# Performance work log

Hardware: AMD Instinct MI355X
Metric: run time of the kernel (lower is better)

## Reference

```python
import jax, jax.numpy as jnp
import numpy as np

B, C, N, T, Hd, L, F = 128, 8, 256, 64, 256, 2, 32  # batch, conv_channels, num_nodes(=hidden), obs_len, hidden, num_layers, filter_num


def setup_inputs() -> dict:
    key = jax.random.key(0)
    ks = jax.random.split(key, 20)
    s = 0.05
    f32 = jnp.float32
    return {
        "x": jax.random.normal(ks[0], (B, C, N, T), f32),
        "wst": jax.random.normal(ks[1], (C,), f32) * s,            # st_conv 1x1 weight
        "bst": jax.random.normal(ks[2], (1,), f32) * s,
        "Wh": jax.random.normal(ks[3], (Hd, N), f32) * s,           # hidden Linear
        "bh": jax.random.normal(ks[4], (Hd,), f32) * s,
        "Wih": jax.random.normal(ks[5], (4 * Hd, Hd), f32) * s,     # LSTM
        "Whh": jax.random.normal(ks[6], (4 * Hd, Hd), f32) * s,
        "bih": jax.random.normal(ks[7], (4 * Hd,), f32) * s,
        "bhh": jax.random.normal(ks[8], (4 * Hd,), f32) * s,
        "Wd": jax.random.normal(ks[9], (Hd, 2 * Hd), f32) * s,      # den Linear(2h->h)
        "bd": jax.random.normal(ks[10], (Hd,), f32) * s,
        "Wc": jax.random.normal(ks[11], (F, T), f32) * s,           # attention conv kernel (filter_num,1,obs_len,1) squeezed
        "bc": jax.random.normal(ks[12], (F,), f32) * s,
        "Wl1": jax.random.normal(ks[13], (F, 2 * Hd), f32) * s,     # attention linear1
        "bl1": jax.random.normal(ks[14], (F,), f32) * s,
        "Wl2": jax.random.normal(ks[15], (Hd, 2 * Hd + F), f32) * s,  # attention linear2
        "bl2": jax.random.normal(ks[16], (Hd,), f32) * s,
        "wend": jax.random.normal(ks[17], (C,), f32) * s,           # end_conv 1x1 weight
        "bend": jax.random.normal(ks[18], (C,), f32) * s,
    }


def _forward(x, wst, bst, Wh, bh, Wih, Whh, bih, bhh, Wd, bd, Wc, bc, Wl1, bl1, Wl2, bl2, wend, bend):
    b = x.shape[0]
    # st_conv (1x1 over channels) + relu, then (B, obs_len, num_nodes)
    y = jax.nn.relu(jnp.einsum("bcnt,c->bnt", x, wst) + bst[0])
    xcon = jax.nn.relu(jnp.einsum("bnt,hn->bth", y, Wh) + bh)  # (B, T, Hd)

    def lstm_cell(xt, ht, ct):
        g = xt @ Wih.T + bih + ht @ Whh.T + bhh
        i, f, gg, o = jnp.split(g, 4, axis=1)
        c2 = jax.nn.sigmoid(f) * ct + jax.nn.sigmoid(i) * jnp.tanh(gg)
        h2 = jax.nn.sigmoid(o) * jnp.tanh(c2)
        return h2, c2

    def attention(Hbuf, htt2):
        # Hbuf: (b, T, Hd); htt2: (b, 2Hd)
        w = htt2 @ Wl1.T + bl1                                   # (b, F)
        cv = jax.nn.relu(jnp.einsum("bto,ft->bof", Hbuf, Wc) + bc)  # (b, Hd, F)
        alpha = jax.nn.sigmoid(jnp.sum(cv * w[:, None, :], axis=2))  # (b, Hd)
        v = jnp.sum(alpha[:, :, None] * cv, axis=1)              # (b, F)
        return jax.nn.relu(jnp.concatenate([htt2, v], axis=1)) @ Wl2.T + bl2

    def step(carry, xt):
        ht, ct, attn_out, Hbuf = carry
        xi = xt
        new_ht = attn_out
        for _ in range(L):
            xd = jnp.concatenate([xi, attn_out], axis=1) @ Wd.T + bd
            ht, ct = lstm_cell(xd, ht, ct)
            htt2 = jnp.concatenate([ct, ht], axis=1)             # (b, 2Hd)
            new_ht = attention(Hbuf, htt2)                       # (b, Hd)
            output = jnp.concatenate([ht, new_ht], axis=1) @ Wd.T + bd
            Hbuf = jax.nn.relu(jnp.concatenate([Hbuf[:, 1:, :], output[:, None, :]], axis=1))
            attn_out = new_ht
            xi = output
        return (ht, ct, attn_out, Hbuf), new_ht

    z = jnp.zeros((b, Hd), x.dtype)
    carry0 = (z, z, z, jnp.zeros((b, T, Hd), x.dtype))
    _, res = jax.lax.scan(step, carry0, jnp.transpose(xcon, (1, 0, 2)))  # (T, b, Hd)
    r = jax.nn.relu(jnp.transpose(res, (1, 2, 0)))              # (b, Hd, T)
    # end_conv 1x1: (b, C, Hd, T)
    return r[:, None, :, :] * wend[None, :, None, None] + bend[None, :, None, None]


def reference(x, wst, bst, Wh, bh, Wih, Whh, bih, bhh, Wd, bd, Wc, bc, Wl1, bl1, Wl2, bl2, wend, bend):
    return _forward(x, wst, bst, Wh, bh, Wih, Whh, bih, bhh, Wd, bd, Wc, bc, Wl1, bl1, Wl2, bl2, wend, bend)
```

## Files before the change

kernel.cpp:

```cpp
#include <hip/hip_runtime.h>
#include <hip/hip_bf16.h>

typedef unsigned int uint;
typedef unsigned short ushort;
typedef __fp16 half2_t __attribute__((ext_vector_type(2)));

__device__ __forceinline__ ushort f16b(float x){
  return __builtin_bit_cast(ushort, (_Float16)x);
}
__device__ __forceinline__ uint pk_rne(float a, float b){
  return (uint)f16b(a) | ((uint)f16b(b) << 16);
}
__device__ __forceinline__ void pk_hl(float a, float b, uint& h, uint& l){
  _Float16 ha = (_Float16)a, hb = (_Float16)b;
  float la = (a - (float)ha) * 2048.f;
  float lb = (b - (float)hb) * 2048.f;
  h = (uint)__builtin_bit_cast(ushort, ha) | ((uint)__builtin_bit_cast(ushort, hb) << 16);
  l = pk_rne(la, lb);
}
__device__ __forceinline__ float fdot2(uint a, uint b, float c){
#if __has_builtin(__builtin_amdgcn_fdot2)
  return __builtin_amdgcn_fdot2(__builtin_bit_cast(half2_t, a),
                                __builtin_bit_cast(half2_t, b), c, false);
#else
  half2_t ha = __builtin_bit_cast(half2_t, a), hb = __builtin_bit_cast(half2_t, b);
  return c + (float)ha.x*(float)hb.x + (float)ha.y*(float)hb.y;
#endif
}
__device__ __forceinline__ float f16sel(uint p, uint hi){
  ushort us = hi ? (ushort)(p >> 16) : (ushort)(p & 0xffffu);
  return (float)__builtin_bit_cast(_Float16, us);
}
__device__ __forceinline__ float sigm(float x){ return 1.0f/(1.0f+__expf(-x)); }
__device__ __forceinline__ float tanh_(float x){
  x = fminf(fmaxf(x, -15.f), 15.f);
  float e = __expf(-2.f*x);
  return (1.f-e)/(1.f+e);
}
#define LO_SCALE (1.0f/2048.0f)


__global__ void kPack(const float* __restrict__ Wd, const float* __restrict__ Wih,
                      const float* __restrict__ Whh, const float* __restrict__ Wl1,
                      const float* __restrict__ Wl2, const float* __restrict__ Wc,
                      const float* __restrict__ Wh,  const float* __restrict__ bih,
                      const float* __restrict__ bhh,
                      uint4* __restrict__ Wd4, uint4* __restrict__ Wc4hi,
                      uint4* __restrict__ Wc4lo, uint4* __restrict__ Wl24,
                      float* __restrict__ Wl1f, uint* __restrict__ Wcrot,
                      uint* __restrict__ WhT2, float* __restrict__ bcomb)
{
  const int NTOT = 32768 + 65536 + 34816 + 16384 + 65536 + 32768 + 1024;
  for (int idx = blockIdx.x*blockDim.x + threadIdx.x; idx < NTOT; idx += gridDim.x*blockDim.x){
    int i = idx;
    if (i < 32768){
      int kpp=i>>8, o=i&255, k0=4*kpp;
      uint h0,l0,h1,l1;
      pk_hl(Wd[o*512+k0],   Wd[o*512+k0+1], h0,l0);
      pk_hl(Wd[o*512+k0+2], Wd[o*512+k0+3], h1,l1);
      Wd4[i] = make_uint4(h0,l0,h1,l1); continue; }
    i -= 32768;
    if (i < 65536){
      int kp=i>>8, hh=i&255;
      uint wh[4], wl[4];
      #pragma unroll
      for (int gi=0; gi<4; gi++){
        int row = gi*256+hh;
        float a,b;
        if (kp<128){ a=Wih[row*256+2*kp]; b=Wih[row*256+2*kp+1]; }
        else       { a=Whh[row*256+2*(kp-128)]; b=Whh[row*256+2*(kp-128)+1]; }
        pk_hl(a,b,wh[gi],wl[gi]);
      }
      Wc4hi[i] = make_uint4(wh[0],wh[1],wh[2],wh[3]);
      Wc4lo[i] = make_uint4(wl[0],wl[1],wl[2],wl[3]); continue; }
    i -= 65536;
    if (i < 34816){
      int kpp=i>>8, o=i&255, k0=4*kpp;
      uint h0,l0,h1,l1;
      pk_hl(Wl2[o*544+k0],   Wl2[o*544+k0+1], h0,l0);
      pk_hl(Wl2[o*544+k0+2], Wl2[o*544+k0+3], h1,l1);
      Wl24[i] = make_uint4(h0,l0,h1,l1); continue; }
    i -= 34816;
    if (i < 16384){ int kk=i>>5, f=i&31; Wl1f[i] = Wl1[f*512+kk]; continue; }
    i -= 16384;
    if (i < 65536){ int bb=i>>10, r=i&1023, ps=r>>5, f=r&31;
      float lo = Wc[f*64 + ((2*ps   - bb) & 63)];
      float hi = Wc[f*64 + ((2*ps+1 - bb) & 63)];
      Wcrot[i] = pk_rne(lo, hi); continue; }
    i -= 65536;
    if (i < 32768){ int np=i>>8, h=i&255;
      WhT2[i] = pk_rne(Wh[h*256+2*np], Wh[h*256+2*np+1]); continue; }
    i -= 32768;
    bcomb[i] = bih[i] + bhh[i];
  }
}

__global__ void k1a(const float* __restrict__ x, const float* __restrict__ wst,
                    const float* __restrict__ bst, ushort* __restrict__ yT)
{
  int b = blockIdx.x, tq = blockIdx.y, n = threadIdx.x;
  float acc[16];
  #pragma unroll
  for (int k=0;k<16;k++) acc[k]=0.f;
  for (int c=0;c<8;c++){
    const float4* xp = (const float4*)(x + ((size_t)((b*8+c)*256 + n)*64 + tq*16));
    float wc = wst[c];
    #pragma unroll
    for (int q=0;q<4;q++){
      float4 v = xp[q];
      acc[4*q+0] += v.x*wc; acc[4*q+1] += v.y*wc;
      acc[4*q+2] += v.z*wc; acc[4*q+3] += v.w*wc;
    }
  }
  float b0 = bst[0];
  #pragma unroll
  for (int k=0;k<16;k++){
    float v = fmaxf(acc[k]+b0, 0.f);
    yT[(size_t)(b*64 + tq*16 + k)*256 + n] = f16b(v);
  }
}

__global__ void k1b(const uint* __restrict__ yT2, const uint* __restrict__ WhT2,
                    const float* __restrict__ bh, float* __restrict__ xcon)
{
  __shared__ uint yp[8192];
  int b = blockIdx.x, tid = threadIdx.x;
  for (int i = tid; i < 8192; i += 256) yp[i] = yT2[(size_t)b*8192 + i];
  __syncthreads();
  int h = tid;
  float bias = bh[h];
  for (int tq=0;tq<4;tq++){
    float acc[16];
    #pragma unroll
    for (int k=0;k<16;k++) acc[k]=0.f;
    for (int np=0;np<128;np++){
      uint w2 = WhT2[np*256 + h];
      #pragma unroll
      for (int k=0;k<16;k++)
        acc[k] = fdot2(yp[(tq*16+k)*128 + np], w2, acc[k]);
    }
    #pragma unroll
    for (int k=0;k<16;k++)
      xcon[(size_t)(b*64 + tq*16 + k)*256 + h] = fmaxf(acc[k]+bias, 0.f);
  }
}

__global__ __launch_bounds__(512, 1)
void TPALSTM_17205638987874_kernel(const float* __restrict__ xcon,
        const uint4* __restrict__ Wd4, const uint4* __restrict__ Wc4hi,
        const uint4* __restrict__ Wc4lo, const uint4* __restrict__ Wl24,
        const float* __restrict__ Wl1f, const uint* __restrict__ Wcrot,
        const float* __restrict__ bd, const float* __restrict__ bcomb,
        const float* __restrict__ bl1, const float* __restrict__ bl2,
        const float* __restrict__ bc, float* __restrict__ res)
{
  __shared__ uint  Hp[32][256];
  __shared__ uint  cvp[256][17];
  __shared__ float gp[8][256];
  __shared__ float p2[2][256];
  __shared__ float ht[256], ct[256], alpha[256], nh[256];
  __shared__ __align__(16) uint2 APR2[288];
  __shared__ uint  wpair[16];

  int b = blockIdx.x, tid = threadIdx.x;
  int g = tid >> 8, o = tid & 255;

  for (int i = tid; i < 32*256; i += 512) ((uint*)Hp)[i] = 0u;
  if (tid < 256){ ht[tid]=0.f; ct[tid]=0.f; }
  if (tid >= 128 && tid < 256) APR2[tid] = make_uint2(0u,0u);
  __syncthreads();

  int base = 0;
  for (int t=0;t<64;t++){
    if (tid < 128){
      const float* xr = xcon + (size_t)(b*64+t)*256;
      uint h,l; pk_hl(xr[2*tid], xr[2*tid+1], h, l);
      APR2[tid] = make_uint2(h,l);
    }
    __syncthreads();

    for (int l=0;l<2;l++){
      {
        float ahi=0.f, alo=0.f;
        const uint4* wp = Wd4 + (size_t)(g*64)*256 + o;
        const uint4* ap = (const uint4*)(APR2 + g*128);
        #pragma unroll 4
        for (int kpp=0;kpp<64;kpp++){
          uint4 w = wp[0]; wp += 256;
          uint4 A = ap[kpp];
          ahi = fdot2(A.x, w.x, ahi); alo = fdot2(A.y, w.x, alo); alo = fdot2(A.x, w.y, alo);
          ahi = fdot2(A.z, w.z, ahi); alo = fdot2(A.w, w.z, alo); alo = fdot2(A.z, w.w, alo);
        }
        p2[g][o] = ahi + alo*LO_SCALE;
      }
      __syncthreads();
      if (tid < 128){
        float x0 = p2[0][2*tid]  + p2[1][2*tid]  + bd[2*tid];
        float x1 = p2[0][2*tid+1]+ p2[1][2*tid+1]+ bd[2*tid+1];
        uint h,l; pk_hl(x0,x1,h,l); APR2[tid]=make_uint2(h,l);
      } else if (tid < 256){
        int j=tid-128; uint h,l; pk_hl(ht[2*j], ht[2*j+1], h, l); APR2[tid]=make_uint2(h,l);
      }
      __syncthreads();
      {
        float ih=0.f,il=0.f,fh=0.f,fl=0.f,gh=0.f,gl=0.f,oh=0.f,ol=0.f;
        const uint4* whp = Wc4hi + (size_t)(g*128)*256 + o;
        const uint4* wlp = Wc4lo + (size_t)(g*128)*256 + o;
        #pragma unroll 2
        for (int kp=g*128; kp<g*128+128; kp++){
          uint4 w = whp[0]; whp += 256;
          uint4 v = wlp[0]; wlp += 256;
          uint2 A = APR2[kp];
          ih=fdot2(A.x,w.x,ih); il=fdot2(A.y,w.x,il); il=fdot2(A.x,v.x,il);
          fh=fdot2(A.x,w.y,fh); fl=fdot2(A.y,w.y,fl); fl=fdot2(A.x,v.y,fl);
          gh=fdot2(A.x,w.z,gh); gl=fdot2(A.y,w.z,gl); gl=fdot2(A.x,v.z,gl);
          oh=fdot2(A.x,w.w,oh); ol=fdot2(A.y,w.w,ol); ol=fdot2(A.x,v.w,ol);
        }
        gp[g*4+0][o]=ih+il*LO_SCALE; gp[g*4+1][o]=fh+fl*LO_SCALE;
        gp[g*4+2][o]=gh+gl*LO_SCALE; gp[g*4+3][o]=oh+ol*LO_SCALE;
      }
      __syncthreads();
      if (g==0){
        float gi = sigm (gp[0][o]+gp[4][o]+bcomb[o]);
        float gf = sigm (gp[1][o]+gp[5][o]+bcomb[256+o]);
        float gg = tanh_(gp[2][o]+gp[6][o]+bcomb[512+o]);
        float go = sigm (gp[3][o]+gp[7][o]+bcomb[768+o]);
        float c2 = gf*ct[o] + gi*gg;
        float h2 = go*tanh_(c2);
        ct[o]=c2; ht[o]=h2;
      }
      __syncthreads();
      if (tid < 128){ uint h,l; pk_hl(fmaxf(ct[2*tid],0.f), fmaxf(ct[2*tid+1],0.f), h,l); APR2[tid]=make_uint2(h,l); }
      else if (tid < 256){ int j=tid-128; uint h,l; pk_hl(fmaxf(ht[2*j],0.f), fmaxf(ht[2*j+1],0.f), h,l); APR2[tid]=make_uint2(h,l); }
      else if (tid < 288){
        int f = tid-256;
        float a=0.f;
        const float* w = Wl1f + f;
        for (int k=0;k<256;k++) a += ct[k]*w[k*32];
        for (int k=0;k<256;k++) a += ht[k]*w[(256+k)*32];
        float wtot = a + bl1[f];
        float wn = __shfl_xor(wtot,1);
        if (!(f&1)) wpair[f>>1] = pk_rne(wtot,wn);
      }
      {
        int rb = base & 63;
        const uint* wr = Wcrot + rb*1024 + g*16;
        float acc[16];
        #pragma unroll
        for (int j=0;j<16;j++) acc[j]=0.f;
        for (int ps=0;ps<32;ps++){
          uint hp = Hp[ps][o];
          const uint* w = wr + ps*32;
          #pragma unroll
          for (int j=0;j<16;j++) acc[j] = fdot2(hp, w[j], acc[j]);
        }
        #pragma unroll
        for (int jj=0;jj<8;jj++){
          int f0 = g*16 + 2*jj;
          cvp[o][g*8+jj] = pk_rne(fmaxf(acc[2*jj]+bc[f0],0.f),
                                  fmaxf(acc[2*jj+1]+bc[f0+1],0.f));
        }
      }
      __syncthreads();
      if (tid < 256){
        float s=0.f;
        #pragma unroll
        for (int p=0;p<16;p++) s = fdot2(cvp[tid][p], wpair[p], s);
        alpha[tid] = sigm(s);
      }
      __syncthreads();
      {
        int og = tid>>5, f = tid&31;
        uint hi = f&1; int fp=f>>1;
        float s=0.f;
        #pragma unroll
        for (int oo=0;oo<16;oo++){
          int oa = og*16+oo;
          s += alpha[oa]*f16sel(cvp[oa][fp], hi);
        }
        ((float*)p2)[og*32+f] = s;
      }
      __syncthreads();
      if (tid<32){
        float v=0.f;
        #pragma unroll
        for (int q=0;q<16;q++) v += ((float*)p2)[q*32+tid];
        float vn = __shfl_xor(v,1);
        if (!(tid&1)){
          uint h,l; pk_hl(fmaxf(v,0.f), fmaxf(vn,0.f), h,l);
          APR2[256+(tid>>1)]=make_uint2(h,l);
        }
      }
      __syncthreads();
      {
        float ahi=0.f, alo=0.f;
        const uint4* wp = Wl24 + (size_t)(g*68)*256 + o;
        const uint4* ap = (const uint4*)(APR2 + g*136);
        #pragma unroll 4
        for (int kpp=0;kpp<68;kpp++){
          uint4 w = wp[0]; wp += 256;
          uint4 A = ap[kpp];
          ahi = fdot2(A.x, w.x, ahi); alo = fdot2(A.y, w.x, alo); alo = fdot2(A.x, w.y, alo);
          ahi = fdot2(A.z, w.z, ahi); alo = fdot2(A.w, w.z, alo); alo = fdot2(A.z, w.w, alo);
        }
        p2[g][o] = ahi + alo*LO_SCALE;
      }
      __syncthreads();
      if (g==0){
        float nhv = p2[0][o]+p2[1][o]+bl2[o];
        nh[o] = nhv;
        if (l==1) res[(size_t)(t*128+b)*256 + o] = nhv;
      }
      __syncthreads();
      if (tid<128){ uint h,l; pk_hl(ht[2*tid], ht[2*tid+1], h,l); APR2[tid]=make_uint2(h,l); }
      else if (tid<256){ int j=tid-128; uint h,l; pk_hl(nh[2*j], nh[2*j+1], h,l); APR2[tid]=make_uint2(h,l); }
      __syncthreads();
      {
        float ahi=0.f, alo=0.f;
        const uint4* wp = Wd4 + (size_t)(g*64)*256 + o;
        const uint4* ap = (const uint4*)(APR2 + g*128);
        #pragma unroll 4
        for (int kpp=0;kpp<64;kpp++){
          uint4 w = wp[0]; wp += 256;
          uint4 A = ap[kpp];
          ahi = fdot2(A.x, w.x, ahi); alo = fdot2(A.y, w.x, alo); alo = fdot2(A.x, w.y, alo);
          ahi = fdot2(A.z, w.z, ahi); alo = fdot2(A.w, w.z, alo); alo = fdot2(A.z, w.w, alo);
        }
        p2[g][o] = ahi + alo*LO_SCALE;
      }
      __syncthreads();
      if (tid<128){
        float u0 = p2[0][2*tid]  + p2[1][2*tid]  + bd[2*tid];
        float u1 = p2[0][2*tid+1]+ p2[1][2*tid+1]+ bd[2*tid+1];
        uint h,l; pk_hl(u0, u1, h, l);
        APR2[tid]=make_uint2(h,l);
        int s = base & 63, ps = s>>1; uint hb = (uint)(s&1);
        uint h0 = (uint)f16b(fmaxf(u0,0.f)), h1 = (uint)f16b(fmaxf(u1,0.f));
        int o0=2*tid, o1=o0+1;
        uint old0 = Hp[ps][o0], old1 = Hp[ps][o1];
        Hp[ps][o0] = hb ? ((old0&0xFFFFu)|(h0<<16)) : ((old0&0xFFFF0000u)|h0);
        Hp[ps][o1] = hb ? ((old1&0xFFFFu)|(h1<<16)) : ((old1&0xFFFF0000u)|h1);
      }
      __syncthreads();
      base++;
    }
  }
}

__global__ void k3(const float* __restrict__ res, const float* __restrict__ wend,
                   const float* __restrict__ bend, float* __restrict__ out)
{
  __shared__ float r2[64][257];
  int b = blockIdx.x, tid = threadIdx.x;
  for (int i = tid; i < 16384; i += 256){
    int t = i >> 8, h = i & 255;
    r2[t][h] = fmaxf(res[(size_t)(t*128+b)*256 + h], 0.f);
  }
  __syncthreads();
  int tt = tid & 63, hg = tid >> 6;
  for (int c=0;c<8;c++){
    float we = wend[c], be = bend[c];
    for (int hh=0;hh<64;hh++){
      int h = hg*64 + hh;
      out[((size_t)(b*8+c)*256 + h)*64 + tt] = r2[tt][h]*we + be;
    }
  }
}

extern "C" __attribute__((visibility("default"), used))
void kernel_launch(void* const* d_in, const int* in_sizes, int n_in,
                   void* d_out, int out_size, void* d_ws, size_t ws_size,
                   hipStream_t stream)
{
  const float* x    = (const float*)d_in[0];
  const float* wst  = (const float*)d_in[1];
  const float* bst  = (const float*)d_in[2];
  const float* Wh   = (const float*)d_in[3];
  const float* bh   = (const float*)d_in[4];
  const float* Wih  = (const float*)d_in[5];
  const float* Whh  = (const float*)d_in[6];
  const float* bih  = (const float*)d_in[7];
  const float* bhh  = (const float*)d_in[8];
  const float* Wd   = (const float*)d_in[9];
  const float* bd   = (const float*)d_in[10];
  const float* Wc   = (const float*)d_in[11];
  const float* bc   = (const float*)d_in[12];
  const float* Wl1  = (const float*)d_in[13];
  const float* bl1  = (const float*)d_in[14];
  const float* Wl2  = (const float*)d_in[15];
  const float* bl2  = (const float*)d_in[16];
  const float* wend = (const float*)d_in[17];
  const float* bend = (const float*)d_in[18];

  char* ws = (char*)d_ws;
  uint4* Wd4   = (uint4*)(ws + 0);
  uint4* Wc4hi = (uint4*)(ws + 524288);
  uint4* Wc4lo = (uint4*)(ws + 1572864);
  uint4* Wl24  = (uint4*)(ws + 2621440);
  float* Wl1f  = (float*)(ws + 3178496);
  uint*  Wcrot = (uint*) (ws + 3244032);
  uint*  WhT2  = (uint*) (ws + 3506176);
  float* bcomb = (float*)(ws + 3637248);
  ushort* yT   = (ushort*)(ws + 3641344);
  float* xcon  = (float*)(ws + 7835648);
  float* res   = (float*)(ws + 16224256);

  kPack<<<512, 256, 0, stream>>>(Wd, Wih, Whh, Wl1, Wl2, Wc, Wh, bih, bhh,
                                 Wd4, Wc4hi, Wc4lo, Wl24, Wl1f, Wcrot, WhT2, bcomb);
  k1a<<<dim3(128,4), 256, 0, stream>>>(x, wst, bst, yT);
  k1b<<<128, 256, 0, stream>>>((const uint*)yT, WhT2, bh, xcon);
  TPALSTM_17205638987874_kernel<<<128, 512, 0, stream>>>(xcon, Wd4, Wc4hi, Wc4lo, Wl24,
                                                         Wl1f, Wcrot, bd, bcomb, bl1, bl2, bc, res);
  k3<<<128, 256, 0, stream>>>(res, wend, bend, (float*)d_out);
}
```

Before: 5.915 ms.

## Double recurrent kernel block to 1024 threads with four-way K-split reductions

Result: faster. 5.108 ms (-13.6%).

```diff
diff --git a/kernel.cpp b/kernel.cpp
--- a/kernel.cpp
+++ b/kernel.cpp
@@ -145,7 +145,7 @@
   }
 }
 
-__global__ __launch_bounds__(512, 1)
+__global__ __launch_bounds__(1024, 1)
 void TPALSTM_17205638987874_kernel(const float* __restrict__ xcon,
         const uint4* __restrict__ Wd4, const uint4* __restrict__ Wc4hi,
         const uint4* __restrict__ Wc4lo, const uint4* __restrict__ Wl24,
@@ -156,16 +156,16 @@
 {
   __shared__ uint  Hp[32][256];
   __shared__ uint  cvp[256][17];
-  __shared__ float gp[8][256];
-  __shared__ float p2[2][256];
-  __shared__ float ht[256], ct[256], alpha[256], nh[256];
+  __shared__ float gp[16][256];
+  __shared__ float p4[4][256];
+  __shared__ float ht[256], ct[256], alpha[256];
   __shared__ __align__(16) uint2 APR2[288];
   __shared__ uint  wpair[16];
 
   int b = blockIdx.x, tid = threadIdx.x;
   int g = tid >> 8, o = tid & 255;
 
-  for (int i = tid; i < 32*256; i += 512) ((uint*)Hp)[i] = 0u;
+  for (int i = tid; i < 32*256; i += 1024) ((uint*)Hp)[i] = 0u;
   if (tid < 256){ ht[tid]=0.f; ct[tid]=0.f; }
   if (tid >= 128 && tid < 256) APR2[tid] = make_uint2(0u,0u);
   __syncthreads();
@@ -182,21 +182,22 @@
     for (int l=0;l<2;l++){
       {
         float ahi=0.f, alo=0.f;
-        const uint4* wp = Wd4 + (size_t)(g*64)*256 + o;
-        const uint4* ap = (const uint4*)(APR2 + g*128);
+        const uint4* wp = Wd4 + (size_t)(g*32)*256 + o;
+        const uint4* ap = (const uint4*)(APR2 + g*64);
         #pragma unroll 4
-        for (int kpp=0;kpp<64;kpp++){
+        for (int kpp=0;kpp<32;kpp++){
           uint4 w = wp[0]; wp += 256;
           uint4 A = ap[kpp];
           ahi = fdot2(A.x, w.x, ahi); alo = fdot2(A.y, w.x, alo); alo = fdot2(A.x, w.y, alo);
           ahi = fdot2(A.z, w.z, ahi); alo = fdot2(A.w, w.z, alo); alo = fdot2(A.z, w.w, alo);
         }
-        p2[g][o] = ahi + alo*LO_SCALE;
+        p4[g][o] = ahi + alo*LO_SCALE;
       }
       __syncthreads();
       if (tid < 128){
-        float x0 = p2[0][2*tid]  + p2[1][2*tid]  + bd[2*tid];
-        float x1 = p2[0][2*tid+1]+ p2[1][2*tid+1]+ bd[2*tid+1];
+        int o0=2*tid, o1=o0+1;
+        float x0 = p4[0][o0]+p4[1][o0]+p4[2][o0]+p4[3][o0]+bd[o0];
+        float x1 = p4[0][o1]+p4[1][o1]+p4[2][o1]+p4[3][o1]+bd[o1];
         uint h,l; pk_hl(x0,x1,h,l); APR2[tid]=make_uint2(h,l);
       } else if (tid < 256){
         int j=tid-128; uint h,l; pk_hl(ht[2*j], ht[2*j+1], h, l); APR2[tid]=make_uint2(h,l);
@@ -204,10 +205,10 @@
       __syncthreads();
       {
         float ih=0.f,il=0.f,fh=0.f,fl=0.f,gh=0.f,gl=0.f,oh=0.f,ol=0.f;
-        const uint4* whp = Wc4hi + (size_t)(g*128)*256 + o;
-        const uint4* wlp = Wc4lo + (size_t)(g*128)*256 + o;
+        const uint4* whp = Wc4hi + (size_t)(g*64)*256 + o;
+        const uint4* wlp = Wc4lo + (size_t)(g*64)*256 + o;
         #pragma unroll 2
-        for (int kp=g*128; kp<g*128+128; kp++){
+        for (int kp=g*64; kp<g*64+64; kp++){
           uint4 w = whp[0]; whp += 256;
           uint4 v = wlp[0]; wlp += 256;
           uint2 A = APR2[kp];
@@ -221,10 +222,10 @@
       }
       __syncthreads();
       if (g==0){
-        float gi = sigm (gp[0][o]+gp[4][o]+bcomb[o]);
-        float gf = sigm (gp[1][o]+gp[5][o]+bcomb[256+o]);
-        float gg = tanh_(gp[2][o]+gp[6][o]+bcomb[512+o]);
-        float go = sigm (gp[3][o]+gp[7][o]+bcomb[768+o]);
+        float gi = sigm (gp[0][o]+gp[4][o]+gp[8][o] +gp[12][o]+bcomb[o]);
+        float gf = sigm (gp[1][o]+gp[5][o]+gp[9][o] +gp[13][o]+bcomb[256+o]);
+        float gg = tanh_(gp[2][o]+gp[6][o]+gp[10][o]+gp[14][o]+bcomb[512+o]);
+        float go = sigm (gp[3][o]+gp[7][o]+gp[11][o]+gp[15][o]+bcomb[768+o]);
         float c2 = gf*ct[o] + gi*gg;
         float h2 = go*tanh_(c2);
         ct[o]=c2; ht[o]=h2;
@@ -232,8 +233,8 @@
       __syncthreads();
       if (tid < 128){ uint h,l; pk_hl(fmaxf(ct[2*tid],0.f), fmaxf(ct[2*tid+1],0.f), h,l); APR2[tid]=make_uint2(h,l); }
       else if (tid < 256){ int j=tid-128; uint h,l; pk_hl(fmaxf(ht[2*j],0.f), fmaxf(ht[2*j+1],0.f), h,l); APR2[tid]=make_uint2(h,l); }
-      else if (tid < 288){
-        int f = tid-256;
+      if (g==2 && o < 32){
+        int f = o;
         float a=0.f;
         const float* w = Wl1f + f;
         for (int k=0;k<256;k++) a += ct[k]*w[k*32];
@@ -242,7 +243,7 @@
         float wn = __shfl_xor(wtot,1);
         if (!(f&1)) wpair[f>>1] = pk_rne(wtot,wn);
       }
-      {
+      if (g < 2){
         int rb = base & 63;
         const uint* wr = Wcrot + rb*1024 + g*16;
         float acc[16];
@@ -274,17 +275,17 @@
         uint hi = f&1; int fp=f>>1;
         float s=0.f;
         #pragma unroll
-        for (int oo=0;oo<16;oo++){
-          int oa = og*16+oo;
+        for (int oo=0;oo<8;oo++){
+          int oa = og*8+oo;
           s += alpha[oa]*f16sel(cvp[oa][fp], hi);
         }
-        ((float*)p2)[og*32+f] = s;
+        ((float*)gp)[og*32+f] = s;
       }
       __syncthreads();
       if (tid<32){
         float v=0.f;
         #pragma unroll
-        for (int q=0;q<16;q++) v += ((float*)p2)[q*32+tid];
+        for (int q=0;q<32;q++) v += ((float*)gp)[q*32+tid];
         float vn = __shfl_xor(v,1);
         if (!(tid&1)){
           uint h,l; pk_hl(fmaxf(v,0.f), fmaxf(vn,0.f), h,l);
@@ -294,49 +295,58 @@
       __syncthreads();
       {
         float ahi=0.f, alo=0.f;
-        const uint4* wp = Wl24 + (size_t)(g*68)*256 + o;
-        const uint4* ap = (const uint4*)(APR2 + g*136);
+        const uint4* wp = Wl24 + (size_t)(g*34)*256 + o;
+        const uint4* ap = (const uint4*)(APR2 + g*68);
         #pragma unroll 4
-        for (int kpp=0;kpp<68;kpp++){
+        for (int kpp=0;kpp<34;kpp++){
           uint4 w = wp[0]; wp += 256;
           uint4 A = ap[kpp];
           ahi = fdot2(A.x, w.x, ahi); alo = fdot2(A.y, w.x, alo); alo = fdot2(A.x, w.y, alo);
           ahi = fdot2(A.z, w.z, ahi); alo = fdot2(A.w, w.z, alo); alo = fdot2(A.z, w.w, alo);
         }
-        p2[g][o] = ahi + alo*LO_SCALE;
-      }
-      __syncthreads();
-      if (g==0){
-        float nhv = p2[0][o]+p2[1][o]+bl2[o];
-        nh[o] = nhv;
-        if (l==1) res[(size_t)(t*128+b)*256 + o] = nhv;
+        p4[g][o] = ahi + alo*LO_SCALE;
       }
       __syncthreads();
       if (tid<128){ uint h,l; pk_hl(ht[2*tid], ht[2*tid+1], h,l); APR2[tid]=make_uint2(h,l); }
-      else if (tid<256){ int j=tid-128; uint h,l; pk_hl(nh[2*j], nh[2*j+1], h,l); APR2[tid]=make_uint2(h,l); }
-      __syncthreads();
+      else if (tid<256){
+        int j=tid-128, o0=2*j, o1=o0+1;
+        float n0 = p4[0][o0]+p4[1][o0]+p4[2][o0]+p4[3][o0]+bl2[o0];
+        float n1 = p4[0][o1]+p4[1][o1]+p4[2][o1]+p4[3][o1]+bl2[o1];
+        uint h,l; pk_hl(n0,n1,h,l); APR2[tid]=make_uint2(h,l);
+        if (l==1){}
+        if (1){
+        }
+        p4[0][o0] = n0; p4[0][o1] = n1;
+      }
+      __syncthreads();
+      if (l==1 && tid>=128 && tid<256){
+        int j=tid-128, o0=2*j, o1=o0+1;
+        float* rr = res + (size_t)(t*128+b)*256;
+        rr[o0] = p4[0][o0]; rr[o1] = p4[0][o1];
+      }
       {
         float ahi=0.f, alo=0.f;
-        const uint4* wp = Wd4 + (size_t)(g*64)*256 + o;
-        const uint4* ap = (const uint4*)(APR2 + g*128);
+        const uint4* wp = Wd4 + (size_t)(g*32)*256 + o;
+        const uint4* ap = (const uint4*)(APR2 + g*64);
         #pragma unroll 4
-        for (int kpp=0;kpp<64;kpp++){
+        for (int kpp=0;kpp<32;kpp++){
           uint4 w = wp[0]; wp += 256;
           uint4 A = ap[kpp];
           ahi = fdot2(A.x, w.x, ahi); alo = fdot2(A.y, w.x, alo); alo = fdot2(A.x, w.y, alo);
           ahi = fdot2(A.z, w.z, ahi); alo = fdot2(A.w, w.z, alo); alo = fdot2(A.z, w.w, alo);
         }
-        p2[g][o] = ahi + alo*LO_SCALE;
+        __syncthreads();
+        p4[g][o] = ahi + alo*LO_SCALE;
       }
       __syncthreads();
       if (tid<128){
-        float u0 = p2[0][2*tid]  + p2[1][2*tid]  + bd[2*tid];
-        float u1 = p2[0][2*tid+1]+ p2[1][2*tid+1]+ bd[2*tid+1];
+        int o0=2*tid, o1=o0+1;
+        float u0 = p4[0][o0]+p4[1][o0]+p4[2][o0]+p4[3][o0]+bd[o0];
+        float u1 = p4[0][o1]+p4[1][o1]+p4[2][o1]+p4[3][o1]+bd[o1];
         uint h,l; pk_hl(u0, u1, h, l);
         APR2[tid]=make_uint2(h,l);
         int s = base & 63, ps = s>>1; uint hb = (uint)(s&1);
         uint h0 = (uint)f16b(fmaxf(u0,0.f)), h1 = (uint)f16b(fmaxf(u1,0.f));
-        int o0=2*tid, o1=o0+1;
         uint old0 = Hp[ps][o0], old1 = Hp[ps][o1];
         Hp[ps][o0] = hb ? ((old0&0xFFFFu)|(h0<<16)) : ((old0&0xFFFF0000u)|h0);
         Hp[ps][o1] = hb ? ((old1&0xFFFFu)|(h1<<16)) : ((old1&0xFFFF0000u)|h1);
@@ -409,7 +419,7 @@
                                  Wd4, Wc4hi, Wc4lo, Wl24, Wl1f, Wcrot, WhT2, bcomb);
   k1a<<<dim3(128,4), 256, 0, stream>>>(x, wst, bst, yT);
   k1b<<<128, 256, 0, stream>>>((const uint*)yT, WhT2, bh, xcon);
-  TPALSTM_17205638987874_kernel<<<128, 512, 0, stream>>>(xcon, Wd4, Wc4hi, Wc4lo, Wl24,
-                                                         Wl1f, Wcrot, bd, bcomb, bl1, bl2, bc, res);
+  TPALSTM_17205638987874_kernel<<<128, 1024, 0, stream>>>(xcon, Wd4, Wc4hi, Wc4lo, Wl24,
+                                                          Wl1f, Wcrot, bd, bcomb, bl1, bl2, bc, res);
   k3<<<128, 256, 0, stream>>>(res, wend, bend, (float*)d_out);
 }
```
